# Kernel optimization log

Hardware: AMD Instinct MI355X
Metric: run time of the kernel (lower is better)

## Reference

```python
import jax, jax.numpy as jnp
import numpy as np

EMBED_DIM = 1024
NUM_HEADS = 16
HEAD_DIM = EMBED_DIM // NUM_HEADS
SCALE = HEAD_DIM ** -0.5


def setup_inputs() -> dict:
    key = jax.random.key(0)
    ks = jax.random.split(key, 12)
    B, S, D = 2, 2048, EMBED_DIM
    w_std = D ** -0.5
    return {
        "query": jax.random.normal(ks[0], (B, S, D), jnp.float32),
        "key": jax.random.normal(ks[1], (B, S, D), jnp.float32),
        "value": jax.random.normal(ks[2], (B, S, D), jnp.float32),
        "mask": jnp.ones((B, S, S), jnp.int32),
        "Wq": jax.random.normal(ks[3], (D, D), jnp.float32) * w_std,
        "bq": jnp.zeros((D,), jnp.float32),
        "Wk": jax.random.normal(ks[4], (D, D), jnp.float32) * w_std,
        "bk": jnp.zeros((D,), jnp.float32),
        "Wv": jax.random.normal(ks[5], (D, D), jnp.float32) * w_std,
        "bv": jnp.zeros((D,), jnp.float32),
        "Wo": jax.random.normal(ks[6], (D, D), jnp.float32) * w_std,
        "bo": jnp.zeros((D,), jnp.float32),
    }


def reference(query, key, value, mask, Wq, bq, Wk, bk, Wv, bv, Wo, bo):
    B, Sq, D = query.shape
    H, Hd = NUM_HEADS, HEAD_DIM
    # projections (torch Linear: x @ W.T + b), then split heads -> [B, H, S, Hd]
    q = (query @ Wq.T + bq).reshape(B, Sq, H, Hd).transpose(0, 2, 1, 3)
    k = (key @ Wk.T + bk).reshape(B, -1, H, Hd).transpose(0, 2, 1, 3)
    v = (value @ Wv.T + bv).reshape(B, -1, H, Hd).transpose(0, 2, 1, 3)
    # scaled dot-product scores [B, H, Sq, Sk]
    scores = jnp.einsum("bhqd,bhkd->bhqk", q, k) * SCALE
    scores = jnp.where(mask[:, None, :, :] == 0, -1e9, scores)
    attn_weights = jax.nn.softmax(scores, axis=-1)
    # dropout rate = 0.0 -> identity in this configuration
    attn_output = jnp.einsum("bhqk,bhkd->bhqd", attn_weights, v)
    attn_output = attn_output.transpose(0, 2, 1, 3).reshape(B, Sq, D)
    output = attn_output @ Wo.T + bo
    return (output, attn_weights)
```

## Files before the change

kernel.cpp:

```cpp
#include <hip/hip_runtime.h>
#include <stdint.h>

#define B_ 2
#define S_ 2048
#define D_ 1024
#define H_ 16
#define HD_ 64
#define NT_ (S_ / 64)
#define SC2_ 0.18033688011112042f

typedef __bf16 bf16_t;
typedef bf16_t bf16x8 __attribute__((ext_vector_type(8)));
typedef float f32x4 __attribute__((ext_vector_type(4)));
typedef unsigned short u16x8 __attribute__((ext_vector_type(8)));
typedef unsigned short u16x4 __attribute__((ext_vector_type(4)));

static __device__ __forceinline__ unsigned short f2b(float f) {
  return __builtin_bit_cast(unsigned short, (bf16_t)f);
}

static __device__ __forceinline__ bf16x8 asb(u16x8 u) {
  return __builtin_bit_cast(bf16x8, u);
}

static __device__ __forceinline__ void barrier_lds() {
  asm volatile("s_waitcnt lgkmcnt(0)" ::: "memory");
  __builtin_amdgcn_s_barrier();
}

__global__ void cast3(const float* __restrict__ a, const float* __restrict__ b,
                      const float* __restrict__ c,
                      unsigned short* __restrict__ dst, int n) {
  const float* src = blockIdx.y == 0 ? a : (blockIdx.y == 1 ? b : c);
  unsigned short* d = dst + (size_t)blockIdx.y * n;
  int i = (blockIdx.x * blockDim.x + threadIdx.x) * 8;
  if (i >= n) return;
  float4 f0 = *(const float4*)(src + i);
  float4 f1 = *(const float4*)(src + i + 4);
  u16x8 o;
  o[0] = f2b(f0.x); o[1] = f2b(f0.y); o[2] = f2b(f0.z); o[3] = f2b(f0.w);
  o[4] = f2b(f1.x); o[5] = f2b(f1.y); o[6] = f2b(f1.z); o[7] = f2b(f1.w);
  *(u16x8*)(d + i) = o;
}

__global__ void cast4(const float* __restrict__ a, const float* __restrict__ b,
                      const float* __restrict__ c, const float* __restrict__ e,
                      unsigned short* __restrict__ dst, int n) {
  const float* src = blockIdx.y == 0 ? a
                   : (blockIdx.y == 1 ? b : (blockIdx.y == 2 ? c : e));
  unsigned short* d = dst + (size_t)blockIdx.y * n;
  int i = (blockIdx.x * blockDim.x + threadIdx.x) * 8;
  if (i >= n) return;
  float4 f0 = *(const float4*)(src + i);
  float4 f1 = *(const float4*)(src + i + 4);
  u16x8 o;
  o[0] = f2b(f0.x); o[1] = f2b(f0.y); o[2] = f2b(f0.z); o[3] = f2b(f0.w);
  o[4] = f2b(f1.x); o[5] = f2b(f1.y); o[6] = f2b(f1.z); o[7] = f2b(f1.w);
  *(u16x8*)(d + i) = o;
}

__global__ void pack_mask(const int* __restrict__ mask,
                          uint32_t* __restrict__ mbits) {
  int i = blockIdx.x * blockDim.x + threadIdx.x;
  unsigned long long bits = __ballot(mask[i] != 0);
  if ((threadIdx.x & 63) == 0)
    *(unsigned long long*)&mbits[i >> 5] = bits;
}

template<int OUTMODE>
__global__ __launch_bounds__(256)
void gemm_bt(const unsigned short* __restrict__ Ab,
             const unsigned short* __restrict__ Wb,
             const float* __restrict__ bq_,
             const float* __restrict__ bk_,
             const float* __restrict__ bv_,
             void* __restrict__ outv,
             int M, int N, int K) {
  const int z = blockIdx.z;
  const unsigned short* A = Ab + (size_t)z * M * K;
  const unsigned short* W = Wb + (size_t)z * N * K;
  const float* bias = z == 0 ? bq_ : (z == 1 ? bk_ : bv_);

  __shared__ __align__(16) unsigned short As[128 * 40];
  __shared__ __align__(16) unsigned short Bs[128 * 40];

  const int tid = threadIdx.x;
  const int lane = tid & 63;
  const int wave = tid >> 6;
  const int wm = wave >> 1, wn = wave & 1;
  const int row0 = blockIdx.x * 128;
  const int col0 = blockIdx.y * 128;

  const int srow = tid >> 2;
  const int scol = (tid & 3) * 8;
  const int lr = lane & 15;
  const int lg = lane >> 4;
  const int lk = lg * 8;

  f32x4 acc[4][4] = {};

  u16x8 a0 = *(const u16x8*)&A[(size_t)(row0 + srow) * K + scol];
  u16x8 a1 = *(const u16x8*)&A[(size_t)(row0 + srow + 64) * K + scol];
  u16x8 b0 = *(const u16x8*)&W[(size_t)(col0 + srow) * K + scol];
  u16x8 b1 = *(const u16x8*)&W[(size_t)(col0 + srow + 64) * K + scol];

  for (int k0 = 0; k0 < K; k0 += 32) {
    barrier_lds();
    *(u16x8*)&As[srow * 40 + scol] = a0;
    *(u16x8*)&As[(srow + 64) * 40 + scol] = a1;
    *(u16x8*)&Bs[srow * 40 + scol] = b0;
    *(u16x8*)&Bs[(srow + 64) * 40 + scol] = b1;
    if (k0 + 32 < K) {
      a0 = *(const u16x8*)&A[(size_t)(row0 + srow) * K + k0 + 32 + scol];
      a1 = *(const u16x8*)&A[(size_t)(row0 + srow + 64) * K + k0 + 32 + scol];
      b0 = *(const u16x8*)&W[(size_t)(col0 + srow) * K + k0 + 32 + scol];
      b1 = *(const u16x8*)&W[(size_t)(col0 + srow + 64) * K + k0 + 32 + scol];
    }
    barrier_lds();

    bf16x8 af[4], bfr[4];
#pragma unroll
    for (int i = 0; i < 4; ++i)
      af[i] = asb(*(const u16x8*)&As[(wm * 64 + i * 16 + lr) * 40 + lk]);
#pragma unroll
    for (int j = 0; j < 4; ++j)
      bfr[j] = asb(*(const u16x8*)&Bs[(wn * 64 + j * 16 + lr) * 40 + lk]);
#pragma unroll
    for (int i = 0; i < 4; ++i)
#pragma unroll
      for (int j = 0; j < 4; ++j)
        acc[i][j] = __builtin_amdgcn_mfma_f32_16x16x32_bf16(af[i], bfr[j], acc[i][j], 0, 0, 0);
  }

  const size_t zo = (size_t)z * M * N;
#pragma unroll
  for (int i = 0; i < 4; ++i) {
#pragma unroll
    for (int j = 0; j < 4; ++j) {
      const int row_ = row0 + wm * 64 + i * 16 + lg * 4;
      const int col = col0 + wn * 64 + j * 16 + lr;
      const float bcol = bias[col];
      if (OUTMODE == 1) {
        float* O = (float*)outv;
#pragma unroll
        for (int r = 0; r < 4; ++r)
          __builtin_nontemporal_store(acc[i][j][r] + bcol,
                                      &O[(size_t)(row_ + r) * N + col]);
      } else if (z == 2) {
        unsigned short* O = (unsigned short*)outv + zo;
        int b = row_ >> 11, s = row_ & 2047;
        int h = col >> 6, hd = col & 63;
        u16x4 pk;
#pragma unroll
        for (int r = 0; r < 4; ++r) pk[r] = f2b(acc[i][j][r] + bcol);
        *(u16x4*)&O[(((size_t)b * H_ + h) * HD_ + hd) * S_ + s] = pk;
      } else {
        unsigned short* O = (unsigned short*)outv + zo;
        int h = col >> 6, hd = col & 63;
#pragma unroll
        for (int r = 0; r < 4; ++r) {
          int row = row_ + r;
          int b = row >> 11, s = row & 2047;
          O[(((size_t)b * H_ + h) * S_ + s) * HD_ + hd] = f2b(acc[i][j][r] + bcol);
        }
      }
    }
  }
}

static __device__ __forceinline__ void xcd_map(int& bh, int& qt) {
  int lin = blockIdx.y * 32 + blockIdx.x;
  int xcd = lin & 7, k = lin >> 3;
  bh = (xcd << 2) | (k >> 5);
  qt = k & 31;
}

__global__ __launch_bounds__(512)
void attn_fused(const unsigned short* __restrict__ q_bh,
                const unsigned short* __restrict__ k_bh,
                const unsigned short* __restrict__ vt_g,
                const uint32_t* __restrict__ mbits,
                float* __restrict__ w_out,
                unsigned short* __restrict__ attn_out) {
  int bh, qt;
  xcd_map(bh, qt);
  const int b = bh >> 4, h = bh & (H_ - 1);
  const int q0 = qt * 64;

  __shared__ __align__(16) unsigned char smem[36864];
  unsigned short* Ks = (unsigned short*)smem;
  unsigned short* Vs = Ks + 64 * 72;
  unsigned short* Kbig = Ks;
  unsigned short* Ps = Vs + 64 * 72;
  float* cs = (float*)smem;
  float2* mls = (float2*)Ps;

  const int tid = threadIdx.x, lane = tid & 63, w = tid >> 6;
  const int wq = w >> 1, wk = w & 1;
  const int srow = tid >> 3, scol = (tid & 7) * 8;
  const int lr = lane & 15, lg = lane >> 4, lk = lg * 8;
  const int sq = q0 + wq * 16 + lr;
  unsigned short* Psw = Ps + w * (16 * 72);

  const unsigned short* qb = q_bh + ((size_t)bh * S_ + sq) * HD_;
  bf16x8 qf0 = asb(*(const u16x8*)&qb[lk]);
  bf16x8 qf1 = asb(*(const u16x8*)&qb[32 + lk]);

  const uint32_t* mrow = mbits + ((size_t)b * S_ + sq) * (S_ / 32);
  const unsigned short* kb = k_bh + (size_t)bh * S_ * HD_;
  const unsigned short* vb = vt_g + (size_t)bh * HD_ * S_;

  float m2 = -__builtin_inff(), l = 0.f;
  {
    u16x8 t0 = *(const u16x8*)&kb[srow * 64 + scol];
    u16x8 t1 = *(const u16x8*)&kb[(srow + 64) * 64 + scol];
    for (int kt = 0; kt < S_ / 128; ++kt) {
      barrier_lds();
      *(u16x8*)&Kbig[srow * 72 + scol] = t0;
      *(u16x8*)&Kbig[(srow + 64) * 72 + scol] = t1;
      if (kt + 1 < S_ / 128) {
        t0 = *(const u16x8*)&kb[((kt + 1) * 128 + srow) * 64 + scol];
        t1 = *(const u16x8*)&kb[((kt + 1) * 128 + 64 + srow) * 64 + scol];
      }
      barrier_lds();

      uint2 mw = *(const uint2*)&mrow[kt * 4 + wk * 2];
      const bool full = __all((mw.x & mw.y) == 0xffffffffu);

      f32x4 sa[4] = {};
#pragma unroll
      for (int j = 0; j < 4; ++j) {
        const int row = wk * 64 + j * 16 + lr;
        bf16x8 kf0 = asb(*(const u16x8*)&Kbig[row * 72 + lk]);
        bf16x8 kf1 = asb(*(const u16x8*)&Kbig[row * 72 + 32 + lk]);
        sa[j] = __builtin_amdgcn_mfma_f32_16x16x32_bf16(kf0, qf0, sa[j], 0, 0, 0);
        sa[j] = __builtin_amdgcn_mfma_f32_16x16x32_bf16(kf1, qf1, sa[j], 0, 0, 0);
      }

      float sv[4][4];
      if (full) {
#pragma unroll
        for (int j = 0; j < 4; ++j)
#pragma unroll
          for (int r = 0; r < 4; ++r) sv[j][r] = sa[j][r] * SC2_;
      } else {
#pragma unroll
        for (int j = 0; j < 4; ++j) {
          uint32_t mwj = (j < 2) ? mw.x : mw.y;
#pragma unroll
          for (int r = 0; r < 4; ++r) {
            int bit = (j & 1) * 16 + lg * 4 + r;
            sv[j][r] = ((mwj >> bit) & 1) ? sa[j][r] * SC2_ : -3.0e9f;
          }
        }
      }
      float tm = sv[0][0];
#pragma unroll
      for (int j = 0; j < 4; ++j)
#pragma unroll
        for (int r = 0; r < 4; ++r) tm = fmaxf(tm, sv[j][r]);
      tm = fmaxf(tm, __shfl_xor(tm, 16));
      tm = fmaxf(tm, __shfl_xor(tm, 32));
      float mnew = fmaxf(m2, tm);
      float ss = 0.f;
#pragma unroll
      for (int j = 0; j < 4; ++j)
#pragma unroll
        for (int r = 0; r < 4; ++r)
          ss += __builtin_amdgcn_exp2f(sv[j][r] - mnew);
      ss += __shfl_xor(ss, 16);
      ss += __shfl_xor(ss, 32);
      l = l * __builtin_amdgcn_exp2f(m2 - mnew) + ss;
      m2 = mnew;
    }
  }

  barrier_lds();
  if (lg == 0) mls[wk * 64 + wq * 16 + lr] = make_float2(m2, l);
  barrier_lds();
  float2 h0 = mls[wq * 16 + lr];
  float2 h1 = mls[64 + wq * 16 + lr];
  const float mn = fmaxf(h0.x, h1.x);
  const float lsum = h0.y * __builtin_amdgcn_exp2f(h0.x - mn) +
                     h1.y * __builtin_amdgcn_exp2f(h1.x - mn);
  const float off = -mn - __builtin_amdgcn_logf(lsum);
  float* wrow = w_out + ((size_t)bh * S_ + sq) * S_;

  u16x8 t0 = *(const u16x8*)&kb[srow * 64 + scol];
  u16x8 v0 = *(const u16x8*)&vb[(size_t)srow * S_ + scol];

  f32x4 oacc[4] = {};

  for (int kt = 0; kt < NT_; ++kt) {
    const int k0 = kt * 64;
    barrier_lds();
    *(u16x8*)&Ks[srow * 72 + scol] = t0;
    *(u16x8*)&Vs[srow * 72 + scol] = v0;
    if (kt + 1 < NT_) {
      t0 = *(const u16x8*)&kb[(k0 + 64 + srow) * 64 + scol];
      v0 = *(const u16x8*)&vb[(size_t)srow * S_ + k0 + 64 + scol];
    }
    barrier_lds();

    uint32_t mw = mrow[kt * 2 + wk];
    const bool full = __all(mw == 0xffffffffu);

    f32x4 sa[2] = {};
#pragma unroll
    for (int jj = 0; jj < 2; ++jj) {
      const int j = wk * 2 + jj;
      bf16x8 kf0 = asb(*(const u16x8*)&Ks[(j * 16 + lr) * 72 + lk]);
      bf16x8 kf1 = asb(*(const u16x8*)&Ks[(j * 16 + lr) * 72 + 32 + lk]);
      sa[jj] = __builtin_amdgcn_mfma_f32_16x16x32_bf16(kf0, qf0, sa[jj], 0, 0, 0);
      sa[jj] = __builtin_amdgcn_mfma_f32_16x16x32_bf16(kf1, qf1, sa[jj], 0, 0, 0);
    }

#pragma unroll
    for (int jj = 0; jj < 2; ++jj) {
      f32x4 pv;
      u16x4 pb;
      if (full) {
#pragma unroll
        for (int r = 0; r < 4; ++r) {
          float p = __builtin_amdgcn_exp2f(fmaf(sa[jj][r], SC2_, off));
          pv[r] = p;
          pb[r] = f2b(p);
        }
      } else {
#pragma unroll
        for (int r = 0; r < 4; ++r) {
          int bit = jj * 16 + lg * 4 + r;
          float x = ((mw >> bit) & 1) ? fmaf(sa[jj][r], SC2_, off) : -3.0e9f;
          float p = __builtin_amdgcn_exp2f(x);
          pv[r] = p;
          pb[r] = f2b(p);
        }
      }
      __builtin_nontemporal_store(pv,
          (f32x4*)&wrow[k0 + wk * 32 + jj * 16 + lg * 4]);
      *(u16x4*)&Psw[lr * 72 + wk * 32 + jj * 16 + lg * 4] = pb;
    }

    bf16x8 pa = asb(*(const u16x8*)&Psw[lr * 72 + wk * 32 + lk]);
#pragma unroll
    for (int j2 = 0; j2 < 4; ++j2) {
      bf16x8 vf = asb(*(const u16x8*)&Vs[(j2 * 16 + lr) * 72 + wk * 32 + lk]);
      oacc[j2] = __builtin_amdgcn_mfma_f32_16x16x32_bf16(pa, vf, oacc[j2], 0, 0, 0);
    }
  }

  barrier_lds();
  const int ci = (wq * 64 + lane) * 17;
  if (wk == 1) {
#pragma unroll
    for (int j2 = 0; j2 < 4; ++j2)
#pragma unroll
      for (int r = 0; r < 4; ++r) cs[ci + j2 * 4 + r] = oacc[j2][r];
  }
  barrier_lds();
  if (wk == 0) {
#pragma unroll
    for (int j2 = 0; j2 < 4; ++j2)
#pragma unroll
      for (int r = 0; r < 4; ++r) {
        float v = oacc[j2][r] + cs[ci + j2 * 4 + r];
        attn_out[((size_t)b * S_ + q0 + wq * 16 + lg * 4 + r) * D_ + h * HD_ + j2 * 16 + lr] =
            f2b(v);
      }
  }
}

extern "C" void kernel_launch(void* const* d_in, const int* in_sizes, int n_in,
                              void* d_out, int out_size, void* d_ws, size_t ws_size,
                              hipStream_t stream) {
  const float* query = (const float*)d_in[0];
  const float* key   = (const float*)d_in[1];
  const float* value = (const float*)d_in[2];
  const int*   mask  = (const int*)d_in[3];
  const float* Wq = (const float*)d_in[4];
  const float* bq = (const float*)d_in[5];
  const float* Wk = (const float*)d_in[6];
  const float* bk = (const float*)d_in[7];
  const float* Wv = (const float*)d_in[8];
  const float* bv = (const float*)d_in[9];
  const float* Wo = (const float*)d_in[10];
  const float* bo = (const float*)d_in[11];

  const int NE = B_ * S_ * D_;
  const int NW = D_ * D_;

  char* ws = (char*)d_ws;
  unsigned short* xin  = (unsigned short*)(ws);
  uint32_t*       mbits = (uint32_t*)(ws + 8388608);
  unsigned short* wbuf = (unsigned short*)(ws + 25165824);
  unsigned short* qkv  = (unsigned short*)(ws + 33554432);
  unsigned short* aout = (unsigned short*)(ws + 59244544);

  cast3<<<dim3(NE / 2048, 3), dim3(256), 0, stream>>>(query, key, value, xin, NE);
  cast4<<<dim3(NW / 2048, 4), dim3(256), 0, stream>>>(Wq, Wk, Wv, Wo, wbuf, NW);

  gemm_bt<0><<<dim3(32, 8, 3), dim3(256), 0, stream>>>(
      xin, wbuf, bq, bk, bv, qkv, 4096, 1024, 1024);

  pack_mask<<<dim3(B_ * S_ * S_ / 256), dim3(256), 0, stream>>>(mask, mbits);

  float* w_out = (float*)d_out + NE;
  attn_fused<<<dim3(32, 32), dim3(512), 0, stream>>>(
      qkv, qkv + NE, qkv + 2 * NE, mbits, w_out, aout);

  gemm_bt<1><<<dim3(32, 8, 1), dim3(256), 0, stream>>>(
      aout, wbuf + 3 * NW, bo, bo, bo, d_out, 4096, 1024, 1024);
}
```

Baseline: 272.4 us.

## Double K/V tile to 128 keys in attention pass and merge cast kernels

The second attention pass now stages 128 keys of K and V per iteration instead of 64, halving the number of barrier-separated loop iterations. Each wave handles two 32-key sub-blocks per iteration, and the per-wave P scratch shrinks to 32 columns. Separately, the two fp32-to-bf16 cast launches are merged into one seven-slice launch to save a kernel launch; weight slices have many idle blocks that exit early. Shared memory grows to 45 KB, which may reduce occupancy for the 512-thread blocks.

```diff
diff --git a/kernel.cpp b/kernel.cpp
--- a/kernel.cpp
+++ b/kernel.cpp
@@ -28,27 +28,26 @@
   __builtin_amdgcn_s_barrier();
 }
 
-__global__ void cast3(const float* __restrict__ a, const float* __restrict__ b,
-                      const float* __restrict__ c,
-                      unsigned short* __restrict__ dst, int n) {
-  const float* src = blockIdx.y == 0 ? a : (blockIdx.y == 1 ? b : c);
-  unsigned short* d = dst + (size_t)blockIdx.y * n;
-  int i = (blockIdx.x * blockDim.x + threadIdx.x) * 8;
-  if (i >= n) return;
-  float4 f0 = *(const float4*)(src + i);
-  float4 f1 = *(const float4*)(src + i + 4);
-  u16x8 o;
-  o[0] = f2b(f0.x); o[1] = f2b(f0.y); o[2] = f2b(f0.z); o[3] = f2b(f0.w);
-  o[4] = f2b(f1.x); o[5] = f2b(f1.y); o[6] = f2b(f1.z); o[7] = f2b(f1.w);
-  *(u16x8*)(d + i) = o;
-}
-
-__global__ void cast4(const float* __restrict__ a, const float* __restrict__ b,
-                      const float* __restrict__ c, const float* __restrict__ e,
-                      unsigned short* __restrict__ dst, int n) {
-  const float* src = blockIdx.y == 0 ? a
-                   : (blockIdx.y == 1 ? b : (blockIdx.y == 2 ? c : e));
-  unsigned short* d = dst + (size_t)blockIdx.y * n;
+__global__ void cast7(const float* __restrict__ q, const float* __restrict__ k,
+                      const float* __restrict__ v, const float* __restrict__ wq,
+                      const float* __restrict__ wk, const float* __restrict__ wv,
+                      const float* __restrict__ wo,
+                      unsigned short* __restrict__ xin,
+                      unsigned short* __restrict__ wbuf,
+                      int ne, int nw) {
+  const int y = blockIdx.y;
+  const float* src;
+  unsigned short* d;
+  int n;
+  if (y < 3) {
+    src = y == 0 ? q : (y == 1 ? k : v);
+    d = xin + (size_t)y * ne;
+    n = ne;
+  } else {
+    src = y == 3 ? wq : (y == 4 ? wk : (y == 5 ? wv : wo));
+    d = wbuf + (size_t)(y - 3) * nw;
+    n = nw;
+  }
   int i = (blockIdx.x * blockDim.x + threadIdx.x) * 8;
   if (i >= n) return;
   float4 f0 = *(const float4*)(src + i);
@@ -187,11 +186,11 @@
   const int b = bh >> 4, h = bh & (H_ - 1);
   const int q0 = qt * 64;
 
-  __shared__ __align__(16) unsigned char smem[36864];
+  __shared__ __align__(16) unsigned char smem[45056];
   unsigned short* Ks = (unsigned short*)smem;
-  unsigned short* Vs = Ks + 64 * 72;
+  unsigned short* Vs = Ks + 128 * 72;
+  unsigned short* Ps = Vs + 64 * 136;
   unsigned short* Kbig = Ks;
-  unsigned short* Ps = Vs + 64 * 72;
   float* cs = (float*)smem;
   float2* mls = (float2*)Ps;
 
@@ -200,7 +199,7 @@
   const int srow = tid >> 3, scol = (tid & 7) * 8;
   const int lr = lane & 15, lg = lane >> 4, lk = lg * 8;
   const int sq = q0 + wq * 16 + lr;
-  unsigned short* Psw = Ps + w * (16 * 72);
+  unsigned short* Psw = Ps + w * (16 * 36);
 
   const unsigned short* qb = q_bh + ((size_t)bh * S_ + sq) * HD_;
   bf16x8 qf0 = asb(*(const u16x8*)&qb[lk]);
@@ -287,65 +286,75 @@
   float* wrow = w_out + ((size_t)bh * S_ + sq) * S_;
 
   u16x8 t0 = *(const u16x8*)&kb[srow * 64 + scol];
+  u16x8 t1 = *(const u16x8*)&kb[(srow + 64) * 64 + scol];
   u16x8 v0 = *(const u16x8*)&vb[(size_t)srow * S_ + scol];
+  u16x8 v1 = *(const u16x8*)&vb[(size_t)srow * S_ + 64 + scol];
 
   f32x4 oacc[4] = {};
 
-  for (int kt = 0; kt < NT_; ++kt) {
-    const int k0 = kt * 64;
+  for (int kt = 0; kt < S_ / 128; ++kt) {
+    const int k0 = kt * 128;
     barrier_lds();
     *(u16x8*)&Ks[srow * 72 + scol] = t0;
-    *(u16x8*)&Vs[srow * 72 + scol] = v0;
-    if (kt + 1 < NT_) {
-      t0 = *(const u16x8*)&kb[(k0 + 64 + srow) * 64 + scol];
-      v0 = *(const u16x8*)&vb[(size_t)srow * S_ + k0 + 64 + scol];
+    *(u16x8*)&Ks[(srow + 64) * 72 + scol] = t1;
+    *(u16x8*)&Vs[srow * 136 + scol] = v0;
+    *(u16x8*)&Vs[srow * 136 + 64 + scol] = v1;
+    if (kt + 1 < S_ / 128) {
+      t0 = *(const u16x8*)&kb[(k0 + 128 + srow) * 64 + scol];
+      t1 = *(const u16x8*)&kb[(k0 + 192 + srow) * 64 + scol];
+      v0 = *(const u16x8*)&vb[(size_t)srow * S_ + k0 + 128 + scol];
+      v1 = *(const u16x8*)&vb[(size_t)srow * S_ + k0 + 192 + scol];
     }
     barrier_lds();
 
-    uint32_t mw = mrow[kt * 2 + wk];
-    const bool full = __all(mw == 0xffffffffu);
-
-    f32x4 sa[2] = {};
-#pragma unroll
-    for (int jj = 0; jj < 2; ++jj) {
-      const int j = wk * 2 + jj;
-      bf16x8 kf0 = asb(*(const u16x8*)&Ks[(j * 16 + lr) * 72 + lk]);
-      bf16x8 kf1 = asb(*(const u16x8*)&Ks[(j * 16 + lr) * 72 + 32 + lk]);
-      sa[jj] = __builtin_amdgcn_mfma_f32_16x16x32_bf16(kf0, qf0, sa[jj], 0, 0, 0);
-      sa[jj] = __builtin_amdgcn_mfma_f32_16x16x32_bf16(kf1, qf1, sa[jj], 0, 0, 0);
-    }
-
-#pragma unroll
-    for (int jj = 0; jj < 2; ++jj) {
-      f32x4 pv;
-      u16x4 pb;
-      if (full) {
-#pragma unroll
-        for (int r = 0; r < 4; ++r) {
-          float p = __builtin_amdgcn_exp2f(fmaf(sa[jj][r], SC2_, off));
-          pv[r] = p;
-          pb[r] = f2b(p);
+#pragma unroll
+    for (int sub = 0; sub < 2; ++sub) {
+      const int cbase = wk * 64 + sub * 32;
+      uint32_t mw = mrow[kt * 4 + wk * 2 + sub];
+      const bool full = __all(mw == 0xffffffffu);
+
+      f32x4 sa[2] = {};
+#pragma unroll
+      for (int jj = 0; jj < 2; ++jj) {
+        const int row = cbase + jj * 16 + lr;
+        bf16x8 kf0 = asb(*(const u16x8*)&Ks[row * 72 + lk]);
+        bf16x8 kf1 = asb(*(const u16x8*)&Ks[row * 72 + 32 + lk]);
+        sa[jj] = __builtin_amdgcn_mfma_f32_16x16x32_bf16(kf0, qf0, sa[jj], 0, 0, 0);
+        sa[jj] = __builtin_amdgcn_mfma_f32_16x16x32_bf16(kf1, qf1, sa[jj], 0, 0, 0);
+      }
+
+#pragma unroll
+      for (int jj = 0; jj < 2; ++jj) {
+        f32x4 pv;
+        u16x4 pb;
+        if (full) {
+#pragma unroll
+          for (int r = 0; r < 4; ++r) {
+            float p = __builtin_amdgcn_exp2f(fmaf(sa[jj][r], SC2_, off));
+            pv[r] = p;
+            pb[r] = f2b(p);
+          }
+        } else {
+#pragma unroll
+          for (int r = 0; r < 4; ++r) {
+            int bit = jj * 16 + lg * 4 + r;
+            float x = ((mw >> bit) & 1) ? fmaf(sa[jj][r], SC2_, off) : -3.0e9f;
+            float p = __builtin_amdgcn_exp2f(x);
+            pv[r] = p;
+            pb[r] = f2b(p);
+          }
         }
-      } else {
-#pragma unroll
-        for (int r = 0; r < 4; ++r) {
-          int bit = jj * 16 + lg * 4 + r;
-          float x = ((mw >> bit) & 1) ? fmaf(sa[jj][r], SC2_, off) : -3.0e9f;
-          float p = __builtin_amdgcn_exp2f(x);
-          pv[r] = p;
-          pb[r] = f2b(p);
-        }
-      }
-      __builtin_nontemporal_store(pv,
-          (f32x4*)&wrow[k0 + wk * 32 + jj * 16 + lg * 4]);
-      *(u16x4*)&Psw[lr * 72 + wk * 32 + jj * 16 + lg * 4] = pb;
-    }
-
-    bf16x8 pa = asb(*(const u16x8*)&Psw[lr * 72 + wk * 32 + lk]);
-#pragma unroll
-    for (int j2 = 0; j2 < 4; ++j2) {
-      bf16x8 vf = asb(*(const u16x8*)&Vs[(j2 * 16 + lr) * 72 + wk * 32 + lk]);
-      oacc[j2] = __builtin_amdgcn_mfma_f32_16x16x32_bf16(pa, vf, oacc[j2], 0, 0, 0);
+        __builtin_nontemporal_store(pv,
+            (f32x4*)&wrow[k0 + cbase + jj * 16 + lg * 4]);
+        *(u16x4*)&Psw[lr * 36 + jj * 16 + lg * 4] = pb;
+      }
+
+      bf16x8 pa = asb(*(const u16x8*)&Psw[lr * 36 + lk]);
+#pragma unroll
+      for (int j2 = 0; j2 < 4; ++j2) {
+        bf16x8 vf = asb(*(const u16x8*)&Vs[(j2 * 16 + lr) * 136 + cbase + lk]);
+        oacc[j2] = __builtin_amdgcn_mfma_f32_16x16x32_bf16(pa, vf, oacc[j2], 0, 0, 0);
+      }
     }
   }
 
@@ -396,8 +405,8 @@
   unsigned short* qkv  = (unsigned short*)(ws + 33554432);
   unsigned short* aout = (unsigned short*)(ws + 59244544);
 
-  cast3<<<dim3(NE / 2048, 3), dim3(256), 0, stream>>>(query, key, value, xin, NE);
-  cast4<<<dim3(NW / 2048, 4), dim3(256), 0, stream>>>(Wq, Wk, Wv, Wo, wbuf, NW);
+  cast7<<<dim3(NE / 2048, 7), dim3(256), 0, stream>>>(
+      query, key, value, Wq, Wk, Wv, Wo, xin, wbuf, NE, NW);
 
   gemm_bt<0><<<dim3(32, 8, 3), dim3(256), 0, stream>>>(
       xin, wbuf, bq, bk, bv, qkv, 4096, 1024, 1024);
```

Result: no change. 270.8 us (-0.6%).
